# Performance work log

Measured on AMD Instinct MI355X. Metric: run time of the kernel, lower is better.

The kernel has to match this reference:

```python
import jax, jax.numpy as jnp
import numpy as np

NUM_TNETS = 8388608
NUM_PINS = 20971520
NUM_NODES = 1048576

def setup_inputs() -> dict:
    key = jax.random.key(0)
    k1, k2, k3 = jax.random.split(key, 3)
    beta = jax.random.uniform(k1, (1,), dtype=jnp.float32)
    tnet_weights = jax.random.uniform(k2, (NUM_TNETS,), dtype=jnp.float32)
    flat_tnet2pin = jax.random.randint(k3, (2 * NUM_TNETS,), 0, NUM_PINS, dtype=jnp.int64)
    pin2node_map = jax.random.randint(jax.random.fold_in(key, 7), (NUM_PINS,), 0, NUM_NODES, dtype=jnp.int64)
    return {
        "beta": beta,
        "tnet_weights": tnet_weights,
        "flat_tnet2pin": flat_tnet2pin,
        "pin2node_map": pin2node_map,
    }

def reference(beta, tnet_weights, flat_tnet2pin, pin2node_map):
    # flat_tnet2pin layout: [src_0, dst_0, src_1, dst_1, ...] (2 pins per timing arc)
    # gather node id for every arc pin: [2*num_tnets]
    node_idx = pin2node_map[flat_tnet2pin]
    # each arc's weight is added at both its source and sink node
    w = jnp.repeat(tnet_weights, 2)  # [w0, w0, w1, w1, ...] matches flat layout
    out = jnp.zeros(NUM_NODES, dtype=jnp.float32).at[node_idx].add(w)
    return out * beta
```

## Files before the change

### kernel.cpp

```cpp
#include <hip/hip_runtime.h>
#include <stdint.h>


#define TILE 4096
#define THREADS 512
#define IPT  8
#define NB1  40
#define SHIFT1 19
#define CAP1R 55296
#define TPB1R 14
#define NB2  64
#define SHIFT2 14
#define CAP2R 34816
#define ACC_NODES 16384
#define PARTS 8
#define CLINE_INTS 16
#define CTRL_BYTES 65536

typedef unsigned long long item_t;
typedef int   int4_ev   __attribute__((ext_vector_type(4)));
typedef float float4_ev __attribute__((ext_vector_type(4)));
typedef unsigned long long ull2_ev __attribute__((ext_vector_type(2)));

__device__ __forceinline__ item_t pack_item(uint32_t key, float w) {
    return (item_t)key | ((item_t)__float_as_uint(w) << 32);
}

__device__ __forceinline__ void multisplit_flush(
    item_t (&e)[IPT], int vcnt, int tile_cnt, int shift,
    int* __restrict__ gcur, int gcur_stride,
    item_t* __restrict__ gout, size_t bin_stride, size_t cap)
{
    __shared__ int hist[256];
    __shared__ unsigned long long combo[256];
    __shared__ int wsum[4];
    __shared__ item_t stage[TILE];
    const int t = threadIdx.x;

    if (t < 256) hist[t] = 0;
    __syncthreads();

    uint32_t rankp[IPT / 2];
#pragma unroll
    for (int k = 0; k < IPT; ++k) {
        int b = (int)((uint32_t)e[k] >> shift);
        uint32_t r = (k < vcnt) ? (uint32_t)atomicAdd(&hist[b], 1) : 0u;
        if ((k & 1) == 0) rankp[k >> 1] = r;
        else              rankp[k >> 1] |= (r << 16);
    }
    __syncthreads();

    int val = (t < 256) ? hist[t] : 0;
    int inc = val;
#pragma unroll
    for (int d = 1; d < 64; d <<= 1) {
        int n = __shfl_up(inc, d, 64);
        if ((t & 63) >= d) inc += n;
    }
    if (t < 256 && (t & 63) == 63) wsum[t >> 6] = inc;
    __syncthreads();
    if (t < 256) {
        int w = t >> 6, prefix = 0;
        if (w > 0) prefix += wsum[0];
        if (w > 1) prefix += wsum[1];
        if (w > 2) prefix += wsum[2];
        int bx = prefix + inc - val;
        int gb = (val > 0) ? atomicAdd(&gcur[t * gcur_stride], val) : 0;
        combo[t] = ((unsigned long long)(uint32_t)gb << 32) | (uint32_t)bx;
    }
    __syncthreads();

#pragma unroll
    for (int k = 0; k < IPT; ++k) {
        if (k < vcnt) {
            int b = (int)((uint32_t)e[k] >> shift);
            int r = (int)((rankp[k >> 1] >> ((k & 1) * 16)) & 0xffffu);
            stage[(int)((uint32_t)combo[b]) + r] = e[k];
        }
    }
    __syncthreads();

    for (int j = t; j < tile_cnt; j += THREADS) {
        item_t ev = stage[j];
        int b = (int)((uint32_t)(ev & 0xffffffffull) >> shift);
        unsigned long long c = combo[b];
        long long dst = (long long)(int)(c >> 32) + (j - (int)(uint32_t)c);
        if (dst >= 0 && dst < (long long)cap)
            __builtin_nontemporal_store(ev, &gout[(size_t)b * bin_stride + (size_t)dst]);
    }
}

__global__ __launch_bounds__(THREADS, 8) void k1_partition_pins(
    const int* __restrict__ flat_pins, const float* __restrict__ weights,
    int* __restrict__ ctrl1, item_t* __restrict__ items1, int total)
{
    const int tileBase = blockIdx.x * TILE;
    const int r = blockIdx.x & 7;
    const int t = threadIdx.x;
    const int base = tileBase + t * IPT;
    item_t e[IPT];
    int vcnt;

    if (base + IPT <= total) {
        vcnt = IPT;
        int4_ev   p[2];
        float4_ev w;
#pragma unroll
        for (int v = 0; v < 2; ++v)
            p[v] = __builtin_nontemporal_load((const int4_ev*)(flat_pins + base) + v);
        w = __builtin_nontemporal_load((const float4_ev*)(weights + (base >> 1)));
#pragma unroll
        for (int k = 0; k < IPT; ++k)
            e[k] = pack_item((uint32_t)p[k >> 2][k & 3], w[(k >> 1) & 3]);
    } else {
        int rem = total - base;
        vcnt = rem < 0 ? 0 : (rem > IPT ? IPT : rem);
#pragma unroll
        for (int k = 0; k < IPT; ++k) {
            int i = base + k;
            bool ok = i < total;
            e[k] = ok ? pack_item((uint32_t)flat_pins[i], weights[i >> 1]) : 0ull;
        }
    }
    int cnt = min(TILE, total - tileBase);
    multisplit_flush(e, vcnt, cnt, SHIFT1,
                     ctrl1 + r * CLINE_INTS, 8 * CLINE_INTS,
                     items1 + (size_t)r * CAP1R, (size_t)8 * CAP1R,
                     (size_t)CAP1R);
}

__global__ __launch_bounds__(THREADS, 8) void k2_gather_partition(
    const item_t* __restrict__ items1, const int* __restrict__ ctrl1,
    const int* __restrict__ pin2node,
    int* __restrict__ ctrl2, item_t* __restrict__ items2)
{
    const int q = blockIdx.x;
    const int r2 = q & 7;
    const int s  = q >> 3;
    const int g    = s / (8 * TPB1R);
    const int rem  = s % (8 * TPB1R);
    const int r_w  = rem / TPB1R;
    const int tile = rem % TPB1R;
    const int bin  = r2 + 8 * g;
    const int cnt = min(ctrl1[(bin * 8 + r_w) * CLINE_INTS], (int)CAP1R);
    const int tbase = tile * TILE;
    if (tbase >= cnt) return;

    const item_t* src = items1 + ((size_t)bin * 8 + (size_t)r_w) * CAP1R;
    const int t = threadIdx.x;
    const int base = tbase + t * IPT;
    item_t e[IPT];
    int vcnt;

    if (base + IPT <= cnt) {
        vcnt = IPT;
        ull2_ev it[4];
#pragma unroll
        for (int v = 0; v < 4; ++v)
            it[v] = __builtin_nontemporal_load((const ull2_ev*)(src + base) + v);
#pragma unroll
        for (int k = 0; k < IPT; ++k) {
            item_t ev = it[k >> 1][k & 1];
            int node = pin2node[(uint32_t)(ev & 0xffffffffull)];
            e[k] = (ev & 0xffffffff00000000ull) | (uint32_t)node;
        }
    } else {
        int rem2 = cnt - base;
        vcnt = rem2 < 0 ? 0 : (rem2 > IPT ? IPT : rem2);
#pragma unroll
        for (int k = 0; k < IPT; ++k) {
            int i = base + k;
            bool ok = i < cnt;
            item_t ev = ok ? src[i] : 0ull;
            int node = ok ? pin2node[(uint32_t)(ev & 0xffffffffull)] : 0;
            e[k] = (ev & 0xffffffff00000000ull) | (uint32_t)node;
        }
    }
    int tcnt = min(TILE, cnt - tbase);
    multisplit_flush(e, vcnt, tcnt, SHIFT2,
                     ctrl2 + r2 * CLINE_INTS, 8 * CLINE_INTS,
                     items2 + (size_t)r2 * CAP2R, (size_t)8 * CAP2R,
                     (size_t)CAP2R);
}

__global__ __launch_bounds__(1024, 8) void k3_accumulate_part(
    const item_t* __restrict__ items2, const int* __restrict__ ctrl2,
    float* __restrict__ partials)
{
    __shared__ float acc[ACC_NODES];
    const int b = blockIdx.x >> 3;
    const int p = blockIdx.x & (PARTS - 1);
    const int t = threadIdx.x;
    for (int i = t; i < ACC_NODES; i += 1024) acc[i] = 0.f;
    __syncthreads();

    const int cnt = min(ctrl2[(b * 8 + p) * CLINE_INTS], (int)CAP2R);
    const item_t* src = items2 + ((size_t)b * 8 + (size_t)p) * CAP2R;

    const int nv = cnt >> 2;
    for (int g = t; g < nv; g += 1024) {
        const item_t* pp = src + ((size_t)g << 2);
        ull2_ev a0 = __builtin_nontemporal_load((const ull2_ev*)pp);
        ull2_ev a1 = __builtin_nontemporal_load((const ull2_ev*)pp + 1);
#pragma unroll
        for (int k = 0; k < 2; ++k) {
            item_t e0 = a0[k], e1 = a1[k];
            atomicAdd(&acc[(uint32_t)(e0 & 0xffffffffull) & (ACC_NODES - 1)],
                      __uint_as_float((uint32_t)(e0 >> 32)));
            atomicAdd(&acc[(uint32_t)(e1 & 0xffffffffull) & (ACC_NODES - 1)],
                      __uint_as_float((uint32_t)(e1 >> 32)));
        }
    }
    for (int i = (nv << 2) + t; i < cnt; i += 1024) {
        item_t e = __builtin_nontemporal_load(&src[i]);
        atomicAdd(&acc[(uint32_t)(e & 0xffffffffull) & (ACC_NODES - 1)],
                  __uint_as_float((uint32_t)(e >> 32)));
    }
    __syncthreads();

    float* __restrict__ dst = partials + (size_t)blockIdx.x * ACC_NODES;
    for (int i = t; i < ACC_NODES; i += 1024) dst[i] = acc[i];
}

__global__ __launch_bounds__(256) void k4_reduce(
    const float* __restrict__ partials, const float* __restrict__ beta,
    float* __restrict__ out, int num_nodes)
{
    const float bt = beta[0];
    const int n = (blockIdx.x * 256 + threadIdx.x) << 2;
    if (n + 3 < num_nodes) {
        const int b   = n >> SHIFT2;
        const int off = n & (ACC_NODES - 1);
        const float* base = partials + ((size_t)b * PARTS) * ACC_NODES + off;
        float4_ev s = {0.f, 0.f, 0.f, 0.f};
#pragma unroll
        for (int p = 0; p < PARTS; ++p)
            s += *(const float4_ev*)(base + (size_t)p * ACC_NODES);
        *(float4_ev*)(out + n) = s * bt;
    } else {
        for (int k = 0; k < 4; ++k) {
            int nn = n + k;
            if (nn < num_nodes) {
                const int b   = nn >> SHIFT2;
                const int off = nn & (ACC_NODES - 1);
                float s = 0.f;
#pragma unroll
                for (int p = 0; p < PARTS; ++p)
                    s += partials[((size_t)b * PARTS + p) * ACC_NODES + off];
                out[nn] = s * bt;
            }
        }
    }
}

__global__ __launch_bounds__(256) void scatter_device(
    const float* __restrict__ beta, const float* __restrict__ tnet_weights,
    const long long* __restrict__ pin_pairs, const int* __restrict__ pin2node_map,
    float* __restrict__ out, int num_tnets)
{
    int t = blockIdx.x * blockDim.x + threadIdx.x;
    if (t >= num_tnets) return;
    long long pp = pin_pairs[t];
    float w = tnet_weights[t] * beta[0];
    atomicAdd(&out[pin2node_map[(int)(pp & 0xffffffffLL)]], w);
    atomicAdd(&out[pin2node_map[(int)(pp >> 32)]], w);
}

extern "C" void kernel_launch(void* const* d_in, const int* in_sizes, int n_in,
                              void* d_out, int out_size, void* d_ws, size_t ws_size,
                              hipStream_t stream) {
    const float* beta         = (const float*)d_in[0];
    const float* weights      = (const float*)d_in[1];
    const int*   flat_pins    = (const int*)d_in[2];
    const int*   pin2node     = (const int*)d_in[3];
    float* out = (float*)d_out;

    const int num_tnets = in_sizes[1];
    const int total     = in_sizes[2];
    const int num_nodes = out_size;

    const size_t items1Bytes = (size_t)NB1 * 8 * CAP1R * sizeof(item_t);
    const size_t items2Bytes = (size_t)NB2 * 8 * CAP2R * sizeof(item_t);
    const size_t partBytes   = (size_t)NB2 * PARTS * ACC_NODES * sizeof(float);

    int* ctrl1 = (int*)d_ws;
    int* ctrl2 = (int*)((char*)d_ws + 32768);
    const int gridTiles = (total + TILE - 1) / TILE;

    if (ws_size >= CTRL_BYTES + items1Bytes + items2Bytes + partBytes) {
        item_t* items1 = (item_t*)((char*)d_ws + CTRL_BYTES);
        item_t* items2 = (item_t*)((char*)d_ws + CTRL_BYTES + items1Bytes);
        float*  partials = (float*)((char*)d_ws + CTRL_BYTES + items1Bytes + items2Bytes);
        (void)hipMemsetAsync(d_ws, 0, CTRL_BYTES, stream);
        k1_partition_pins<<<gridTiles, THREADS, 0, stream>>>(
            flat_pins, weights, ctrl1, items1, total);
        k2_gather_partition<<<NB1 * 8 * TPB1R, THREADS, 0, stream>>>(
            items1, ctrl1, pin2node, ctrl2, items2);
        k3_accumulate_part<<<NB2 * PARTS, 1024, 0, stream>>>(
            items2, ctrl2, partials);
        const int i4slots = (num_nodes + 3) / 4;
        k4_reduce<<<(i4slots + 255) / 256, 256, 0, stream>>>(
            partials, beta, out, num_nodes);
    } else {
        (void)hipMemsetAsync(d_out, 0, (size_t)out_size * sizeof(float), stream);
        scatter_device<<<(num_tnets + 255) / 256, 256, 0, stream>>>(
            beta, weights, (const long long*)flat_pins, pin2node, out, num_tnets);
    }
}
```

Baseline: 433.1 us.

## Make partition kernels persistent with ticket work stealing and prefetch next tile

k1 and k2 now launch a fixed grid of 1024 blocks that pull tiles from per-residue atomic ticket counters and loop. Each iteration issues the global loads for the next tile before the scatter-out of the current tile, overlapping load latency with stores. Barriers become raw s_barrier with explicit lgkmcnt waits, and the histogram reset is folded into the scan. k3 now software-pipelines its loads with double-buffered registers across four strided quarters. The cost is extra atomics, more register pressure, and persistent-loop control complexity.

New measurement: 464.6 us. 7.3% more time.

```diff
diff --git a/kernel.cpp b/kernel.cpp
--- a/kernel.cpp
+++ b/kernel.cpp
@@ -15,41 +15,38 @@
 #define ACC_NODES 16384
 #define PARTS 8
 #define CLINE_INTS 16
-#define CTRL_BYTES 65536
+#define TICK1_OFF 65536
+#define TICK2_OFF 66048
+#define CTRL_BYTES 66560
+#define NT2R (5 * 8 * TPB1R)
 
 typedef unsigned long long item_t;
 typedef int   int4_ev   __attribute__((ext_vector_type(4)));
 typedef float float4_ev __attribute__((ext_vector_type(4)));
 typedef unsigned long long ull2_ev __attribute__((ext_vector_type(2)));
 
+#define BAR() do { __builtin_amdgcn_sched_barrier(0); \
+    asm volatile("s_waitcnt lgkmcnt(0)" ::: "memory"); \
+    __builtin_amdgcn_s_barrier(); \
+    __builtin_amdgcn_sched_barrier(0); } while (0)
+
 __device__ __forceinline__ item_t pack_item(uint32_t key, float w) {
     return (item_t)key | ((item_t)__float_as_uint(w) << 32);
 }
 
-__device__ __forceinline__ void multisplit_flush(
-    item_t (&e)[IPT], int vcnt, int tile_cnt, int shift,
-    int* __restrict__ gcur, int gcur_stride,
-    item_t* __restrict__ gout, size_t bin_stride, size_t cap)
-{
-    __shared__ int hist[256];
-    __shared__ unsigned long long combo[256];
-    __shared__ int wsum[4];
-    __shared__ item_t stage[TILE];
-    const int t = threadIdx.x;
-
-    if (t < 256) hist[t] = 0;
-    __syncthreads();
-
-    uint32_t rankp[IPT / 2];
+__device__ __forceinline__ void ms_passA(item_t (&e)[IPT], int vcnt, int shift,
+                                         int* hist, uint32_t (&rankp)[IPT / 2]) {
 #pragma unroll
     for (int k = 0; k < IPT; ++k) {
         int b = (int)((uint32_t)e[k] >> shift);
-        uint32_t r = (k < vcnt) ? (uint32_t)atomicAdd(&hist[b], 1) : 0u;
-        if ((k & 1) == 0) rankp[k >> 1] = r;
-        else              rankp[k >> 1] |= (r << 16);
-    }
-    __syncthreads();
-
+        uint32_t rr = (k < vcnt) ? (uint32_t)atomicAdd(&hist[b], 1) : 0u;
+        if ((k & 1) == 0) rankp[k >> 1] = rr;
+        else              rankp[k >> 1] |= (rr << 16);
+    }
+}
+
+__device__ __forceinline__ void ms_scan(int t, int* hist, unsigned long long* combo,
+                                        int* wsum, int* gcur, int gcur_stride) {
     int val = (t < 256) ? hist[t] : 0;
     int inc = val;
 #pragma unroll
@@ -58,8 +55,9 @@
         if ((t & 63) >= d) inc += n;
     }
     if (t < 256 && (t & 63) == 63) wsum[t >> 6] = inc;
-    __syncthreads();
+    BAR();
     if (t < 256) {
+        hist[t] = 0;
         int w = t >> 6, prefix = 0;
         if (w > 0) prefix += wsum[0];
         if (w > 1) prefix += wsum[1];
@@ -68,18 +66,24 @@
         int gb = (val > 0) ? atomicAdd(&gcur[t * gcur_stride], val) : 0;
         combo[t] = ((unsigned long long)(uint32_t)gb << 32) | (uint32_t)bx;
     }
-    __syncthreads();
-
+}
+
+__device__ __forceinline__ void ms_passD(item_t (&e)[IPT], int vcnt, int shift,
+                                         uint32_t (&rankp)[IPT / 2],
+                                         unsigned long long* combo, item_t* stage) {
 #pragma unroll
     for (int k = 0; k < IPT; ++k) {
         if (k < vcnt) {
             int b = (int)((uint32_t)e[k] >> shift);
-            int r = (int)((rankp[k >> 1] >> ((k & 1) * 16)) & 0xffffu);
-            stage[(int)((uint32_t)combo[b]) + r] = e[k];
-        }
-    }
-    __syncthreads();
-
+            int rr = (int)((rankp[k >> 1] >> ((k & 1) * 16)) & 0xffffu);
+            stage[(int)((uint32_t)combo[b]) + rr] = e[k];
+        }
+    }
+}
+
+__device__ __forceinline__ void ms_passE(int t, item_t* stage, int tile_cnt, int shift,
+                                         unsigned long long* combo,
+                                         item_t* gout, size_t bin_stride, size_t cap) {
     for (int j = t; j < tile_cnt; j += THREADS) {
         item_t ev = stage[j];
         int b = (int)((uint32_t)(ev & 0xffffffffull) >> shift);
@@ -92,95 +96,215 @@
 
 __global__ __launch_bounds__(THREADS, 8) void k1_partition_pins(
     const int* __restrict__ flat_pins, const float* __restrict__ weights,
-    int* __restrict__ ctrl1, item_t* __restrict__ items1, int total)
+    int* __restrict__ ctrl1, int* __restrict__ tick1,
+    item_t* __restrict__ items1, int total)
 {
-    const int tileBase = blockIdx.x * TILE;
+    __shared__ int hist[256];
+    __shared__ unsigned long long combo[256];
+    __shared__ int wsum[4];
+    __shared__ item_t stage[TILE];
+    __shared__ int sh_tk;
+
+    const int t = threadIdx.x;
     const int r = blockIdx.x & 7;
-    const int t = threadIdx.x;
-    const int base = tileBase + t * IPT;
+    const int gridTiles = (total + TILE - 1) / TILE;
+    const int ntr = (gridTiles > r) ? ((gridTiles - r + 7) >> 3) : 0;
+    int* mytick = tick1 + r * CLINE_INTS;
+    int* mycur  = ctrl1 + r * CLINE_INTS;
+    item_t* mout = items1 + (size_t)r * CAP1R;
+
+    if (t == 0) sh_tk = atomicAdd(mytick, 1);
+    if (t < 256) hist[t] = 0;
+    __syncthreads();
+    if (sh_tk >= ntr) return;
+
     item_t e[IPT];
-    int vcnt;
-
-    if (base + IPT <= total) {
-        vcnt = IPT;
-        int4_ev   p[2];
-        float4_ev w;
-#pragma unroll
-        for (int v = 0; v < 2; ++v)
-            p[v] = __builtin_nontemporal_load((const int4_ev*)(flat_pins + base) + v);
-        w = __builtin_nontemporal_load((const float4_ev*)(weights + (base >> 1)));
-#pragma unroll
-        for (int k = 0; k < IPT; ++k)
-            e[k] = pack_item((uint32_t)p[k >> 2][k & 3], w[(k >> 1) & 3]);
-    } else {
-        int rem = total - base;
-        vcnt = rem < 0 ? 0 : (rem > IPT ? IPT : rem);
-#pragma unroll
-        for (int k = 0; k < IPT; ++k) {
-            int i = base + k;
-            bool ok = i < total;
-            e[k] = ok ? pack_item((uint32_t)flat_pins[i], weights[i >> 1]) : 0ull;
-        }
-    }
-    int cnt = min(TILE, total - tileBase);
-    multisplit_flush(e, vcnt, cnt, SHIFT1,
-                     ctrl1 + r * CLINE_INTS, 8 * CLINE_INTS,
-                     items1 + (size_t)r * CAP1R, (size_t)8 * CAP1R,
-                     (size_t)CAP1R);
+    int vcnt, tcnt;
+    {
+        int tb = (r + (sh_tk << 3)) * TILE;
+        int base = tb + t * IPT;
+        tcnt = min(TILE, total - tb);
+        if (base + IPT <= total) {
+            vcnt = IPT;
+            int4_ev p0 = __builtin_nontemporal_load((const int4_ev*)(flat_pins + base));
+            int4_ev p1 = __builtin_nontemporal_load((const int4_ev*)(flat_pins + base) + 1);
+            float4_ev w = __builtin_nontemporal_load((const float4_ev*)(weights + (base >> 1)));
+#pragma unroll
+            for (int k = 0; k < IPT; ++k)
+                e[k] = pack_item((uint32_t)((k < 4) ? p0[k & 3] : p1[k & 3]), w[(k >> 1) & 3]);
+        } else {
+            int rem = total - base;
+            vcnt = rem < 0 ? 0 : (rem > IPT ? IPT : rem);
+#pragma unroll
+            for (int k = 0; k < IPT; ++k) {
+                int i = base + k;
+                e[k] = (i < total) ? pack_item((uint32_t)flat_pins[i], weights[i >> 1]) : 0ull;
+            }
+        }
+    }
+    __syncthreads();
+
+    for (;;) {
+        int tkf = 0x7fffffff;
+        if (t == 0) tkf = atomicAdd(mytick, 1);
+        uint32_t rankp[IPT / 2];
+        ms_passA(e, vcnt, SHIFT1, hist, rankp);
+        BAR();
+        ms_scan(t, hist, combo, wsum, mycur, 8 * CLINE_INTS);
+        if (t == 0) sh_tk = tkf;
+        BAR();
+        ms_passD(e, vcnt, SHIFT1, rankp, combo, stage);
+        BAR();
+        const int tkn = sh_tk;
+        const bool valid = (tkn < ntr);
+        int4_ev px0, px1; float4_ev wx;
+        bool fastN = false; int baseN = 0, tbN = 0;
+        if (valid) {
+            tbN = (r + (tkn << 3)) * TILE;
+            baseN = tbN + t * IPT;
+            fastN = (baseN + IPT <= total);
+            if (fastN) {
+                px0 = __builtin_nontemporal_load((const int4_ev*)(flat_pins + baseN));
+                px1 = __builtin_nontemporal_load((const int4_ev*)(flat_pins + baseN) + 1);
+                wx  = __builtin_nontemporal_load((const float4_ev*)(weights + (baseN >> 1)));
+            }
+        }
+        ms_passE(t, stage, tcnt, SHIFT1, combo, mout, (size_t)8 * CAP1R, (size_t)CAP1R);
+        BAR();
+        if (!valid) break;
+        tcnt = min(TILE, total - tbN);
+        if (fastN) {
+            vcnt = IPT;
+#pragma unroll
+            for (int k = 0; k < IPT; ++k)
+                e[k] = pack_item((uint32_t)((k < 4) ? px0[k & 3] : px1[k & 3]), wx[(k >> 1) & 3]);
+        } else {
+            int rem = total - baseN;
+            vcnt = rem < 0 ? 0 : (rem > IPT ? IPT : rem);
+#pragma unroll
+            for (int k = 0; k < IPT; ++k) {
+                int i = baseN + k;
+                e[k] = (i < total) ? pack_item((uint32_t)flat_pins[i], weights[i >> 1]) : 0ull;
+            }
+        }
+    }
 }
 
 __global__ __launch_bounds__(THREADS, 8) void k2_gather_partition(
     const item_t* __restrict__ items1, const int* __restrict__ ctrl1,
-    const int* __restrict__ pin2node,
-    int* __restrict__ ctrl2, item_t* __restrict__ items2)
+    const int* __restrict__ pin2node, int* __restrict__ ctrl2,
+    int* __restrict__ tick2, item_t* __restrict__ items2)
 {
-    const int q = blockIdx.x;
-    const int r2 = q & 7;
-    const int s  = q >> 3;
-    const int g    = s / (8 * TPB1R);
-    const int rem  = s % (8 * TPB1R);
-    const int r_w  = rem / TPB1R;
-    const int tile = rem % TPB1R;
-    const int bin  = r2 + 8 * g;
-    const int cnt = min(ctrl1[(bin * 8 + r_w) * CLINE_INTS], (int)CAP1R);
-    const int tbase = tile * TILE;
-    if (tbase >= cnt) return;
-
-    const item_t* src = items1 + ((size_t)bin * 8 + (size_t)r_w) * CAP1R;
+    __shared__ int hist[256];
+    __shared__ unsigned long long combo[256];
+    __shared__ int wsum[4];
+    __shared__ item_t stage[TILE];
+    __shared__ int sh_tk;
+    __shared__ int sh_cnt[NB1];
+
     const int t = threadIdx.x;
-    const int base = tbase + t * IPT;
+    const int r2 = blockIdx.x & 7;
+    int* mytick = tick2 + r2 * CLINE_INTS;
+    int* mycur  = ctrl2 + r2 * CLINE_INTS;
+    item_t* mout = items2 + (size_t)r2 * CAP2R;
+
+    if (t == 0) sh_tk = atomicAdd(mytick, 1);
+    if (t < 256) hist[t] = 0;
+    if (t < NB1) {
+        int bin = r2 + 8 * (t >> 3);
+        sh_cnt[t] = min(ctrl1[(bin * 8 + (t & 7)) * CLINE_INTS], (int)CAP1R);
+    }
+    __syncthreads();
+    if (sh_tk >= NT2R) return;
+
+#define GMERGE(slot, ev_) { item_t ev = (ev_); \
+        int nd = pin2node[(uint32_t)ev]; \
+        e[slot] = (ev & 0xffffffff00000000ull) | (uint32_t)nd; }
+
     item_t e[IPT];
-    int vcnt;
-
-    if (base + IPT <= cnt) {
-        vcnt = IPT;
-        ull2_ev it[4];
-#pragma unroll
-        for (int v = 0; v < 4; ++v)
-            it[v] = __builtin_nontemporal_load((const ull2_ev*)(src + base) + v);
-#pragma unroll
-        for (int k = 0; k < IPT; ++k) {
-            item_t ev = it[k >> 1][k & 1];
-            int node = pin2node[(uint32_t)(ev & 0xffffffffull)];
-            e[k] = (ev & 0xffffffff00000000ull) | (uint32_t)node;
-        }
-    } else {
-        int rem2 = cnt - base;
-        vcnt = rem2 < 0 ? 0 : (rem2 > IPT ? IPT : rem2);
-#pragma unroll
-        for (int k = 0; k < IPT; ++k) {
-            int i = base + k;
-            bool ok = i < cnt;
-            item_t ev = ok ? src[i] : 0ull;
-            int node = ok ? pin2node[(uint32_t)(ev & 0xffffffffull)] : 0;
-            e[k] = (ev & 0xffffffff00000000ull) | (uint32_t)node;
-        }
-    }
-    int tcnt = min(TILE, cnt - tbase);
-    multisplit_flush(e, vcnt, tcnt, SHIFT2,
-                     ctrl2 + r2 * CLINE_INTS, 8 * CLINE_INTS,
-                     items2 + (size_t)r2 * CAP2R, (size_t)8 * CAP2R,
-                     (size_t)CAP2R);
+    int vcnt, tcnt;
+    {
+        int tk = sh_tk;
+        int g = tk / (8 * TPB1R), rem = tk % (8 * TPB1R);
+        int r_w = rem / TPB1R, tile = rem % TPB1R;
+        int bin = r2 + 8 * g;
+        int cnt = sh_cnt[(g << 3) | r_w];
+        int tb = tile * TILE;
+        tcnt = max(0, min(TILE, cnt - tb));
+        const item_t* src = items1 + ((size_t)bin * 8 + (size_t)r_w) * CAP1R;
+        int base = tb + t * IPT;
+        if (base + IPT <= cnt) {
+            vcnt = IPT;
+            ull2_ev x0 = __builtin_nontemporal_load((const ull2_ev*)(src + base));
+            ull2_ev x1 = __builtin_nontemporal_load((const ull2_ev*)(src + base) + 1);
+            ull2_ev x2 = __builtin_nontemporal_load((const ull2_ev*)(src + base) + 2);
+            ull2_ev x3 = __builtin_nontemporal_load((const ull2_ev*)(src + base) + 3);
+            GMERGE(0, x0[0]) GMERGE(1, x0[1]) GMERGE(2, x1[0]) GMERGE(3, x1[1])
+            GMERGE(4, x2[0]) GMERGE(5, x2[1]) GMERGE(6, x3[0]) GMERGE(7, x3[1])
+        } else {
+            int rem2 = cnt - base;
+            vcnt = rem2 < 0 ? 0 : (rem2 > IPT ? IPT : rem2);
+#pragma unroll
+            for (int k = 0; k < IPT; ++k) {
+                int i = base + k;
+                if (i >= 0 && i < cnt) { GMERGE(k, src[i]) } else e[k] = 0ull;
+            }
+        }
+    }
+    __syncthreads();
+
+    for (;;) {
+        int tkf = 0x7fffffff;
+        if (t == 0) tkf = atomicAdd(mytick, 1);
+        uint32_t rankp[IPT / 2];
+        ms_passA(e, vcnt, SHIFT2, hist, rankp);
+        BAR();
+        ms_scan(t, hist, combo, wsum, mycur, 8 * CLINE_INTS);
+        if (t == 0) sh_tk = tkf;
+        BAR();
+        ms_passD(e, vcnt, SHIFT2, rankp, combo, stage);
+        BAR();
+        const int tkn = sh_tk;
+        const bool valid = (tkn < NT2R);
+        ull2_ev nx0, nx1, nx2, nx3;
+        bool fastN = false;
+        const item_t* srcN = items1;
+        int baseN = 0, cntN = 0, tbN = 0;
+        if (valid) {
+            int g = tkn / (8 * TPB1R), rem = tkn % (8 * TPB1R);
+            int r_w = rem / TPB1R, tile = rem % TPB1R;
+            int bin = r2 + 8 * g;
+            cntN = sh_cnt[(g << 3) | r_w];
+            tbN = tile * TILE;
+            srcN = items1 + ((size_t)bin * 8 + (size_t)r_w) * CAP1R;
+            baseN = tbN + t * IPT;
+            fastN = (baseN + IPT <= cntN);
+            if (fastN) {
+                nx0 = __builtin_nontemporal_load((const ull2_ev*)(srcN + baseN));
+                nx1 = __builtin_nontemporal_load((const ull2_ev*)(srcN + baseN) + 1);
+                nx2 = __builtin_nontemporal_load((const ull2_ev*)(srcN + baseN) + 2);
+                nx3 = __builtin_nontemporal_load((const ull2_ev*)(srcN + baseN) + 3);
+            }
+        }
+        ms_passE(t, stage, tcnt, SHIFT2, combo, mout, (size_t)8 * CAP2R, (size_t)CAP2R);
+        BAR();
+        if (!valid) break;
+        tcnt = max(0, min(TILE, cntN - tbN));
+        if (fastN) {
+            vcnt = IPT;
+            GMERGE(0, nx0[0]) GMERGE(1, nx0[1]) GMERGE(2, nx1[0]) GMERGE(3, nx1[1])
+            GMERGE(4, nx2[0]) GMERGE(5, nx2[1]) GMERGE(6, nx3[0]) GMERGE(7, nx3[1])
+        } else {
+            int rem2 = cntN - baseN;
+            vcnt = rem2 < 0 ? 0 : (rem2 > IPT ? IPT : rem2);
+#pragma unroll
+            for (int k = 0; k < IPT; ++k) {
+                int i = baseN + k;
+                if (i >= 0 && i < cntN) { GMERGE(k, srcN[i]) } else e[k] = 0ull;
+            }
+        }
+    }
+#undef GMERGE
 }
 
 __global__ __launch_bounds__(1024, 8) void k3_accumulate_part(
@@ -196,28 +320,44 @@
 
     const int cnt = min(ctrl2[(b * 8 + p) * CLINE_INTS], (int)CAP2R);
     const item_t* src = items2 + ((size_t)b * 8 + (size_t)p) * CAP2R;
-
-    const int nv = cnt >> 2;
-    for (int g = t; g < nv; g += 1024) {
-        const item_t* pp = src + ((size_t)g << 2);
-        ull2_ev a0 = __builtin_nontemporal_load((const ull2_ev*)pp);
-        ull2_ev a1 = __builtin_nontemporal_load((const ull2_ev*)pp + 1);
-#pragma unroll
-        for (int k = 0; k < 2; ++k) {
-            item_t e0 = a0[k], e1 = a1[k];
-            atomicAdd(&acc[(uint32_t)(e0 & 0xffffffffull) & (ACC_NODES - 1)],
-                      __uint_as_float((uint32_t)(e0 >> 32)));
-            atomicAdd(&acc[(uint32_t)(e1 & 0xffffffffull) & (ACC_NODES - 1)],
-                      __uint_as_float((uint32_t)(e1 >> 32)));
-        }
-    }
-    for (int i = (nv << 2) + t; i < cnt; i += 1024) {
-        item_t e = __builtin_nontemporal_load(&src[i]);
-        atomicAdd(&acc[(uint32_t)(e & 0xffffffffull) & (ACC_NODES - 1)],
-                  __uint_as_float((uint32_t)(e >> 32)));
-    }
-    __syncthreads();
-
+    const ull2_ev* src2 = (const ull2_ev*)src;
+    const int npair = cnt >> 1;
+    const int quarter = npair >> 2;
+
+#define K3_LOAD(A0, A1, A2, A3, g) { \
+    A0 = __builtin_nontemporal_load(src2 + (g)); \
+    A1 = __builtin_nontemporal_load(src2 + quarter + (g)); \
+    A2 = __builtin_nontemporal_load(src2 + 2 * quarter + (g)); \
+    A3 = __builtin_nontemporal_load(src2 + 3 * quarter + (g)); }
+#define K3_ACC1(ev) atomicAdd(&acc[(uint32_t)(ev) & (ACC_NODES - 1)], \
+                              __uint_as_float((uint32_t)((ev) >> 32)))
+#define K3_PROC(A0, A1, A2, A3) { \
+    K3_ACC1(A0[0]); K3_ACC1(A0[1]); K3_ACC1(A1[0]); K3_ACC1(A1[1]); \
+    K3_ACC1(A2[0]); K3_ACC1(A2[1]); K3_ACC1(A3[0]); K3_ACC1(A3[1]); }
+
+    ull2_ev a0, a1, a2, a3, b0, b1, b2, b3;
+    int g = t;
+    bool vA = g < quarter;
+    if (vA) K3_LOAD(a0, a1, a2, a3, g)
+    int gB = g + 1024;
+    while (vA) {
+        bool vB = gB < quarter;
+        if (vB) K3_LOAD(b0, b1, b2, b3, gB)
+        K3_PROC(a0, a1, a2, a3)
+        g = gB + 1024;
+        vA = g < quarter;
+        if (vA) K3_LOAD(a0, a1, a2, a3, g)
+        if (vB) K3_PROC(b0, b1, b2, b3)
+        gB = g + 1024;
+    }
+    for (int i = (quarter << 3) + t; i < cnt; i += 1024) {
+        item_t ev = src[i];
+        K3_ACC1(ev);
+    }
+#undef K3_LOAD
+#undef K3_ACC1
+#undef K3_PROC
+    __syncthreads();
     float* __restrict__ dst = partials + (size_t)blockIdx.x * ACC_NODES;
     for (int i = t; i < ACC_NODES; i += 1024) dst[i] = acc[i];
 }
@@ -285,17 +425,18 @@
 
     int* ctrl1 = (int*)d_ws;
     int* ctrl2 = (int*)((char*)d_ws + 32768);
-    const int gridTiles = (total + TILE - 1) / TILE;
+    int* tick1 = (int*)((char*)d_ws + TICK1_OFF);
+    int* tick2 = (int*)((char*)d_ws + TICK2_OFF);
 
     if (ws_size >= CTRL_BYTES + items1Bytes + items2Bytes + partBytes) {
         item_t* items1 = (item_t*)((char*)d_ws + CTRL_BYTES);
         item_t* items2 = (item_t*)((char*)d_ws + CTRL_BYTES + items1Bytes);
         float*  partials = (float*)((char*)d_ws + CTRL_BYTES + items1Bytes + items2Bytes);
         (void)hipMemsetAsync(d_ws, 0, CTRL_BYTES, stream);
-        k1_partition_pins<<<gridTiles, THREADS, 0, stream>>>(
-            flat_pins, weights, ctrl1, items1, total);
-        k2_gather_partition<<<NB1 * 8 * TPB1R, THREADS, 0, stream>>>(
-            items1, ctrl1, pin2node, ctrl2, items2);
+        k1_partition_pins<<<1024, THREADS, 0, stream>>>(
+            flat_pins, weights, ctrl1, tick1, items1, total);
+        k2_gather_partition<<<1024, THREADS, 0, stream>>>(
+            items1, ctrl1, pin2node, ctrl2, tick2, items2);
         k3_accumulate_part<<<NB2 * PARTS, 1024, 0, stream>>>(
             items2, ctrl2, partials);
         const int i4slots = (num_nodes + 3) / 4;
```
